# Optimization experiments

Measured on AMD Instinct MI355X. Metric: run time of the kernel, lower is better.

Reference implementation:

```python
import jax, jax.numpy as jnp
import numpy as np

B, N, DIM, K, H, R = 128, 196, 384, 16, 6, 4  # batch, tokens, channels, bases, heads, adapter ratio


def setup_inputs() -> dict:
    key = jax.random.key(0)
    ks = jax.random.split(key, 4)
    d_r = DIM // R
    return {
        "x": jax.random.normal(ks[0], (B, N, DIM), jnp.float32),
        "W1": jax.random.normal(ks[1], (DIM, d_r), jnp.float32) * 0.02,
        "b1": jnp.zeros((d_r,), jnp.float32),
        "W2": jax.random.normal(ks[2], (d_r, K * H), jnp.float32) * 0.02,
        "b2": jnp.zeros((K * H,), jnp.float32),
        "weight_bank": jax.random.normal(ks[3], (K, N, N), jnp.float32) * 0.02,
    }


def reference(x, W1, b1, W2, b2, weight_bank):
    Bsz, n, C = x.shape
    hdim = C // H
    # adapter MLP: Linear -> GELU(exact/erf, torch default) -> Linear
    hid = jax.nn.gelu(x @ W1 + b1, approximate=False)
    mix = (hid @ W2 + b2).reshape(Bsz, n, K, H)
    # mode='softmax': normalize mixing policy over the k bases
    mix = jax.nn.softmax(mix, axis=2)
    # dynamic per-sample token-mixing matrix [B, n, n, H]
    weight = jnp.einsum('bnkh,knm->bnmh', mix, weight_bank)
    # mix tokens: contract over source token index n
    xh = x.reshape(Bsz, n, H, hdim)
    out = jnp.einsum('bnhc,bnmh->bmhc', xh, weight).reshape(Bsz, n, C)
    return out
```

## Files before the change

kernel.cpp:

```cpp
#include <hip/hip_runtime.h>
#include <math.h>

#define BB  128
#define NN  196
#define CDIM 384
#define KK  16
#define HH  6
#define DR  96
#define HD  64

typedef __attribute__((ext_vector_type(8))) short bf16x8;
typedef __attribute__((ext_vector_type(4))) float f32x4;

__device__ __forceinline__ unsigned short f2bf(float f) {
    unsigned u = __float_as_uint(f);
    u += 0x7FFFu + ((u >> 16) & 1u);
    return (unsigned short)(u >> 16);
}
__device__ __forceinline__ unsigned pk2bf(float lo, float hi) {
    return (unsigned)f2bf(lo) | ((unsigned)f2bf(hi) << 16);
}
__device__ __forceinline__ float bflo(unsigned u) { return __uint_as_float(u << 16); }
__device__ __forceinline__ float bfhi(unsigned u) { return __uint_as_float(u & 0xFFFF0000u); }

union AFrag { unsigned u[4]; bf16x8 f; };

__global__ __launch_bounds__(128) void prep_kernel(
    const float* __restrict__ W1, const float* __restrict__ W2,
    unsigned short* __restrict__ W1T, unsigned short* __restrict__ W2T)
{
    const int c = blockIdx.x;
    const int t = threadIdx.x;
    for (int k = t; k < CDIM; k += 128)
        W1T[(size_t)c * CDIM + k] = f2bf(W1[(size_t)k * DR + c]);
    if (t < DR)
        W2T[(size_t)c * DR + t] = f2bf(W2[(size_t)t * DR + c]);
}

__global__ __launch_bounds__(256, 3) void adapter_kernel(
    const float* __restrict__ x,   const unsigned short* __restrict__ W1T,
    const float* __restrict__ b1,  const unsigned short* __restrict__ W2T,
    const float* __restrict__ b2,  unsigned short* __restrict__ mix_out)
{
    __shared__ unsigned short hidb[32][104];

    const int t    = threadIdx.x;
    const int w    = t >> 6;
    const int wm   = w & 1;
    const int wc   = w >> 1;
    const int lane = t & 63;
    const int l15  = lane & 15;
    const int lq   = lane >> 4;
    const int row0 = blockIdx.x * 32;

    f32x4 acc[3];
    #pragma unroll
    for (int ct = 0; ct < 3; ++ct) {
        const float bj = b1[wc * 48 + ct * 16 + l15];
        acc[ct] = (f32x4){bj, bj, bj, bj};
    }
    const float* xrow = x + (size_t)(row0 + wm * 16 + l15) * CDIM;
    for (int kc = 0; kc < CDIM; kc += 32) {
        const float4 u = *(const float4*)(xrow + kc + 8 * lq);
        const float4 v = *(const float4*)(xrow + kc + 8 * lq + 4);
        AFrag af;
        af.u[0] = pk2bf(u.x, u.y); af.u[1] = pk2bf(u.z, u.w);
        af.u[2] = pk2bf(v.x, v.y); af.u[3] = pk2bf(v.z, v.w);
        #pragma unroll
        for (int ct = 0; ct < 3; ++ct) {
            const bf16x8 bf = *(const bf16x8*)(W1T + (size_t)(wc * 48 + ct * 16 + l15) * CDIM + kc + 8 * lq);
            acc[ct] = __builtin_amdgcn_mfma_f32_16x16x32_bf16(af.f, bf, acc[ct], 0, 0, 0);
        }
    }
    #pragma unroll
    for (int ct = 0; ct < 3; ++ct)
        #pragma unroll
        for (int r = 0; r < 4; ++r) {
            const float vv = acc[ct][r];
            hidb[wm * 16 + lq * 4 + r][wc * 48 + ct * 16 + l15] =
                f2bf(0.5f * vv * (1.0f + erff(vv * 0.70710678118654752f)));
        }
    __syncthreads();

    f32x4 acc2[3];
    #pragma unroll
    for (int ct = 0; ct < 3; ++ct) {
        const float bj = b2[wc * 48 + ct * 16 + l15];
        acc2[ct] = (f32x4){bj, bj, bj, bj};
    }
    #pragma unroll
    for (int kc = 0; kc < DR; kc += 32) {
        const bf16x8 af = *(const bf16x8*)&hidb[wm * 16 + l15][kc + 8 * lq];
        #pragma unroll
        for (int ct = 0; ct < 3; ++ct) {
            const bf16x8 bf = *(const bf16x8*)(W2T + (size_t)(wc * 48 + ct * 16 + l15) * DR + kc + 8 * lq);
            acc2[ct] = __builtin_amdgcn_mfma_f32_16x16x32_bf16(af, bf, acc2[ct], 0, 0, 0);
        }
    }
    __syncthreads();

    #pragma unroll
    for (int ct = 0; ct < 3; ++ct)
        #pragma unroll
        for (int r = 0; r < 4; ++r)
            hidb[wm * 16 + lq * 4 + r][wc * 48 + ct * 16 + l15] = f2bf(acc2[ct][r]);
    __syncthreads();

    if (t < 192) {
        const int r = t / 6, h = t % 6;
        float lg[KK];
        float mx = -1e30f;
        #pragma unroll
        for (int k = 0; k < KK; ++k) {
            lg[k] = __uint_as_float((unsigned)hidb[r][6 * k + h] << 16);
            mx = fmaxf(mx, lg[k]);
        }
        float s = 0.f;
        #pragma unroll
        for (int k = 0; k < KK; ++k) { lg[k] = __expf(lg[k] - mx); s += lg[k]; }
        const float inv = 1.0f / s;
        unsigned o[8];
        #pragma unroll
        for (int jj = 0; jj < 8; ++jj)
            o[jj] = pk2bf(lg[2 * jj] * inv, lg[2 * jj + 1] * inv);
        unsigned* op = (unsigned*)(mix_out + ((size_t)(row0 + r) * HH + h) * KK);
        *(uint4*)op       = make_uint4(o[0], o[1], o[2], o[3]);
        *(uint4*)(op + 4) = make_uint4(o[4], o[5], o[6], o[7]);
    }
}

__global__ __launch_bounds__(384, 3) void mix_mfma_kernel(
    const float* __restrict__ x,  const unsigned short* __restrict__ mixb,
    const float* __restrict__ wb, float* __restrict__ out)
{
    __shared__ unsigned short xT[CDIM][40];
    __shared__ unsigned short Asb[HH][64][40];
    __shared__ unsigned short msc[32][96];

    const int t   = threadIdx.x;
    const int bid = blockIdx.x;
    const int q   = bid & 3;
    const int b   = bid >> 2;
    const int m0  = q * 52;
    const int qvalid = (q == 3) ? 40 : 52;
    const int h   = t >> 6;
    const int lane = t & 63;
    const int l15 = lane & 15;
    const int lq  = lane >> 4;

    f32x4 acc[4][4];
    #pragma unroll
    for (int mt = 0; mt < 4; ++mt)
        #pragma unroll
        for (int ct = 0; ct < 4; ++ct) acc[mt][ct] = (f32x4){0.f, 0.f, 0.f, 0.f};

    for (int nc = 0; nc < 7; ++nc) {
        const int n0 = nc * 32;
        __syncthreads();

        #pragma unroll
        for (int it = 0; it < 4; ++it) {
            const int task = t + 384 * it;
            const int p  = task & 15;
            const int cq = task >> 4;
            const int n  = n0 + 2 * p;
            float4 va = make_float4(0.f, 0.f, 0.f, 0.f);
            float4 vb = make_float4(0.f, 0.f, 0.f, 0.f);
            if (n < NN)     va = *(const float4*)(x + ((size_t)b * NN + n) * CDIM + 4 * cq);
            if (n + 1 < NN) vb = *(const float4*)(x + ((size_t)b * NN + n + 1) * CDIM + 4 * cq);
            *(unsigned*)&xT[4 * cq + 0][2 * p] = pk2bf(va.x, vb.x);
            *(unsigned*)&xT[4 * cq + 1][2 * p] = pk2bf(va.y, vb.y);
            *(unsigned*)&xT[4 * cq + 2][2 * p] = pk2bf(va.z, vb.z);
            *(unsigned*)&xT[4 * cq + 3][2 * p] = pk2bf(va.w, vb.w);
        }
        #pragma unroll
        for (int it = 0; it < 4; ++it) {
            const int idx = t + 384 * it;
            const int nl = idx / 48, cw = idx - nl * 48;
            unsigned v = 0u;
            if (n0 + nl < NN)
                v = *(const unsigned*)(mixb + ((size_t)b * NN + n0 + nl) * DR + 2 * cw);
            *(unsigned*)&msc[nl][2 * cw] = v;
        }
        __syncthreads();

        for (int task = t; task < 832; task += 384) {
            const int nl = task / 26;
            const int mp = task - nl * 26;
            const int n  = n0 + nl;
            const int ms = 2 * mp;
            if (n < NN && ms < qvalid) {
                const int m = m0 + ms;
                float2 wv[KK];
                #pragma unroll
                for (int k = 0; k < KK; ++k)
                    wv[k] = *(const float2*)(wb + ((size_t)k * NN + n) * NN + m);
                #pragma unroll
                for (int hh = 0; hh < HH; ++hh) {
                    const uint4 u = *(const uint4*)&msc[nl][hh * 16];
                    const uint4 v = *(const uint4*)&msc[nl][hh * 16 + 8];
                    const unsigned uu[8] = {u.x, u.y, u.z, u.w, v.x, v.y, v.z, v.w};
                    float a0 = 0.f, a1 = 0.f;
                    #pragma unroll
                    for (int p = 0; p < 8; ++p) {
                        const float f0 = bflo(uu[p]), f1 = bfhi(uu[p]);
                        a0 += f0 * wv[2 * p].x;     a1 += f0 * wv[2 * p].y;
                        a0 += f1 * wv[2 * p + 1].x; a1 += f1 * wv[2 * p + 1].y;
                    }
                    Asb[hh][ms][nl]     = f2bf(a0);
                    Asb[hh][ms + 1][nl] = f2bf(a1);
                }
            } else {
                #pragma unroll
                for (int hh = 0; hh < HH; ++hh) {
                    Asb[hh][ms][nl] = 0; Asb[hh][ms + 1][nl] = 0;
                }
            }
        }
        __syncthreads();

        bf16x8 afr[4], bfr[4];
        #pragma unroll
        for (int mt = 0; mt < 4; ++mt)
            afr[mt] = *(const bf16x8*)&Asb[h][mt * 16 + l15][8 * lq];
        #pragma unroll
        for (int ct = 0; ct < 4; ++ct)
            bfr[ct] = *(const bf16x8*)&xT[h * HD + ct * 16 + l15][8 * lq];
        #pragma unroll
        for (int mt = 0; mt < 4; ++mt)
            #pragma unroll
            for (int ct = 0; ct < 4; ++ct)
                acc[mt][ct] = __builtin_amdgcn_mfma_f32_16x16x32_bf16(
                    afr[mt], bfr[ct], acc[mt][ct], 0, 0, 0);
    }

    #pragma unroll
    for (int mt = 0; mt < 4; ++mt) {
        #pragma unroll
        for (int r = 0; r < 4; ++r) {
            const int ms = mt * 16 + lq * 4 + r;
            if (ms < qvalid) {
                float* op = out + ((size_t)b * NN + m0 + ms) * CDIM + h * HD + l15;
                #pragma unroll
                for (int ct = 0; ct < 4; ++ct)
                    op[ct * 16] = acc[mt][ct][r];
            }
        }
    }
}

extern "C" void kernel_launch(void* const* d_in, const int* in_sizes, int n_in,
                              void* d_out, int out_size, void* d_ws, size_t ws_size,
                              hipStream_t stream) {
    (void)in_sizes; (void)n_in; (void)out_size; (void)ws_size;
    const float* x  = (const float*)d_in[0];
    const float* W1 = (const float*)d_in[1];
    const float* b1 = (const float*)d_in[2];
    const float* W2 = (const float*)d_in[3];
    const float* b2 = (const float*)d_in[4];
    const float* wb = (const float*)d_in[5];
    float* out = (float*)d_out;

    unsigned short* mixbuf = (unsigned short*)d_ws;
    unsigned short* w1t = (unsigned short*)((char*)d_ws + 4816896);
    unsigned short* w2t = (unsigned short*)((char*)d_ws + 4890624);

    prep_kernel<<<96, 128, 0, stream>>>(W1, W2, w1t, w2t);
    adapter_kernel<<<(BB * NN) / 32, 256, 0, stream>>>(x, w1t, b1, w2t, b2, mixbuf);
    mix_mfma_kernel<<<4 * BB, 384, 0, stream>>>(x, mixbuf, wb, out);
}
```

Baseline: 224.4 us.

## Compute dynamic mixing weights with MFMA from a transposed bf16 weight bank

```diff
diff --git a/kernel.cpp b/kernel.cpp
--- a/kernel.cpp
+++ b/kernel.cpp
@@ -20,38 +20,54 @@
 __device__ __forceinline__ unsigned pk2bf(float lo, float hi) {
     return (unsigned)f2bf(lo) | ((unsigned)f2bf(hi) << 16);
 }
-__device__ __forceinline__ float bflo(unsigned u) { return __uint_as_float(u << 16); }
-__device__ __forceinline__ float bfhi(unsigned u) { return __uint_as_float(u & 0xFFFF0000u); }
 
 union AFrag { unsigned u[4]; bf16x8 f; };
 
-__global__ __launch_bounds__(128) void prep_kernel(
+__global__ __launch_bounds__(256) void prep_kernel(
     const float* __restrict__ W1, const float* __restrict__ W2,
-    unsigned short* __restrict__ W1T, unsigned short* __restrict__ W2T)
+    const float* __restrict__ wb,
+    unsigned short* __restrict__ W1T, unsigned short* __restrict__ W2T,
+    unsigned short* __restrict__ wbT)
 {
-    const int c = blockIdx.x;
-    const int t = threadIdx.x;
-    for (int k = t; k < CDIM; k += 128)
-        W1T[(size_t)c * CDIM + k] = f2bf(W1[(size_t)k * DR + c]);
-    if (t < DR)
-        W2T[(size_t)c * DR + t] = f2bf(W2[(size_t)t * DR + c]);
-}
-
-__global__ __launch_bounds__(256, 3) void adapter_kernel(
+    const int bid = blockIdx.x;
+    const int t   = threadIdx.x;
+    if (bid < DR) {
+        const int c = bid;
+        for (int k = t; k < CDIM; k += 256)
+            W1T[(size_t)c * CDIM + k] = f2bf(W1[(size_t)k * DR + c]);
+        if (t < DR)
+            W2T[(size_t)c * DR + t] = f2bf(W2[(size_t)t * DR + c]);
+    } else {
+        const int n = bid - DR;
+        const int m = t;
+        if (m < NN) {
+            unsigned o[8];
+            #pragma unroll
+            for (int j = 0; j < 8; ++j) {
+                const float a = wb[((size_t)(2 * j)     * NN + n) * NN + m];
+                const float c = wb[((size_t)(2 * j + 1) * NN + n) * NN + m];
+                o[j] = pk2bf(a, c);
+            }
+            unsigned* dst = (unsigned*)(wbT + ((size_t)n * NN + m) * KK);
+            *(uint4*)dst       = make_uint4(o[0], o[1], o[2], o[3]);
+            *(uint4*)(dst + 4) = make_uint4(o[4], o[5], o[6], o[7]);
+        }
+    }
+}
+
+__global__ __launch_bounds__(128, 3) void adapter_kernel(
     const float* __restrict__ x,   const unsigned short* __restrict__ W1T,
     const float* __restrict__ b1,  const unsigned short* __restrict__ W2T,
     const float* __restrict__ b2,  unsigned short* __restrict__ mix_out)
 {
-    __shared__ unsigned short hidb[32][104];
+    __shared__ unsigned short hidb[16][104];
 
     const int t    = threadIdx.x;
-    const int w    = t >> 6;
-    const int wm   = w & 1;
-    const int wc   = w >> 1;
+    const int wc   = t >> 6;
     const int lane = t & 63;
     const int l15  = lane & 15;
     const int lq   = lane >> 4;
-    const int row0 = blockIdx.x * 32;
+    const int row0 = blockIdx.x * 16;
 
     f32x4 acc[3];
     #pragma unroll
@@ -59,7 +75,7 @@
         const float bj = b1[wc * 48 + ct * 16 + l15];
         acc[ct] = (f32x4){bj, bj, bj, bj};
     }
-    const float* xrow = x + (size_t)(row0 + wm * 16 + l15) * CDIM;
+    const float* xrow = x + (size_t)(row0 + l15) * CDIM;
     for (int kc = 0; kc < CDIM; kc += 32) {
         const float4 u = *(const float4*)(xrow + kc + 8 * lq);
         const float4 v = *(const float4*)(xrow + kc + 8 * lq + 4);
@@ -77,7 +93,7 @@
         #pragma unroll
         for (int r = 0; r < 4; ++r) {
             const float vv = acc[ct][r];
-            hidb[wm * 16 + lq * 4 + r][wc * 48 + ct * 16 + l15] =
+            hidb[lq * 4 + r][wc * 48 + ct * 16 + l15] =
                 f2bf(0.5f * vv * (1.0f + erff(vv * 0.70710678118654752f)));
         }
     __syncthreads();
@@ -90,7 +106,7 @@
     }
     #pragma unroll
     for (int kc = 0; kc < DR; kc += 32) {
-        const bf16x8 af = *(const bf16x8*)&hidb[wm * 16 + l15][kc + 8 * lq];
+        const bf16x8 af = *(const bf16x8*)&hidb[l15][kc + 8 * lq];
         #pragma unroll
         for (int ct = 0; ct < 3; ++ct) {
             const bf16x8 bf = *(const bf16x8*)(W2T + (size_t)(wc * 48 + ct * 16 + l15) * DR + kc + 8 * lq);
@@ -103,10 +119,10 @@
     for (int ct = 0; ct < 3; ++ct)
         #pragma unroll
         for (int r = 0; r < 4; ++r)
-            hidb[wm * 16 + lq * 4 + r][wc * 48 + ct * 16 + l15] = f2bf(acc2[ct][r]);
+            hidb[lq * 4 + r][wc * 48 + ct * 16 + l15] = f2bf(acc2[ct][r]);
     __syncthreads();
 
-    if (t < 192) {
+    if (t < 96) {
         const int r = t / 6, h = t % 6;
         float lg[KK];
         float mx = -1e30f;
@@ -129,30 +145,36 @@
     }
 }
 
-__global__ __launch_bounds__(384, 3) void mix_mfma_kernel(
+__global__ __launch_bounds__(192, 3) void mix_mfma_kernel(
     const float* __restrict__ x,  const unsigned short* __restrict__ mixb,
-    const float* __restrict__ wb, float* __restrict__ out)
+    const unsigned short* __restrict__ wbT, float* __restrict__ out)
 {
-    __shared__ unsigned short xT[CDIM][40];
-    __shared__ unsigned short Asb[HH][64][40];
-    __shared__ unsigned short msc[32][96];
-
-    const int t   = threadIdx.x;
-    const int bid = blockIdx.x;
-    const int q   = bid & 3;
-    const int b   = bid >> 2;
-    const int m0  = q * 52;
+    __shared__ unsigned short xT[192][40];
+    __shared__ unsigned short Asb[3][64][40];
+
+    const int t    = threadIdx.x;
+    const int bid  = blockIdx.x;
+    const int b    = bid & 127;
+    const int sub  = bid >> 7;
+    const int q    = sub >> 1;
+    const int hp   = sub & 1;
+    const int m0   = q * 52;
     const int qvalid = (q == 3) ? 40 : 52;
-    const int h   = t >> 6;
+    const int lw   = t >> 6;
+    const int hbase = hp * 3;
     const int lane = t & 63;
-    const int l15 = lane & 15;
-    const int lq  = lane >> 4;
+    const int l15  = lane & 15;
+    const int lq   = lane >> 4;
+    const int c0   = hp * 192;
+
+    const bf16x8 z8 = {0, 0, 0, 0, 0, 0, 0, 0};
+    const f32x4  cz = {0.f, 0.f, 0.f, 0.f};
 
     f32x4 acc[4][4];
     #pragma unroll
     for (int mt = 0; mt < 4; ++mt)
         #pragma unroll
-        for (int ct = 0; ct < 4; ++ct) acc[mt][ct] = (f32x4){0.f, 0.f, 0.f, 0.f};
+        for (int ct = 0; ct < 4; ++ct) acc[mt][ct] = cz;
 
     for (int nc = 0; nc < 7; ++nc) {
         const int n0 = nc * 32;
@@ -160,61 +182,49 @@
 
         #pragma unroll
         for (int it = 0; it < 4; ++it) {
-            const int task = t + 384 * it;
+            const int task = t + 192 * it;
             const int p  = task & 15;
             const int cq = task >> 4;
             const int n  = n0 + 2 * p;
             float4 va = make_float4(0.f, 0.f, 0.f, 0.f);
             float4 vb = make_float4(0.f, 0.f, 0.f, 0.f);
-            if (n < NN)     va = *(const float4*)(x + ((size_t)b * NN + n) * CDIM + 4 * cq);
-            if (n + 1 < NN) vb = *(const float4*)(x + ((size_t)b * NN + n + 1) * CDIM + 4 * cq);
+            if (n < NN)     va = *(const float4*)(x + ((size_t)b * NN + n) * CDIM + c0 + 4 * cq);
+            if (n + 1 < NN) vb = *(const float4*)(x + ((size_t)b * NN + n + 1) * CDIM + c0 + 4 * cq);
             *(unsigned*)&xT[4 * cq + 0][2 * p] = pk2bf(va.x, vb.x);
             *(unsigned*)&xT[4 * cq + 1][2 * p] = pk2bf(va.y, vb.y);
             *(unsigned*)&xT[4 * cq + 2][2 * p] = pk2bf(va.z, vb.z);
             *(unsigned*)&xT[4 * cq + 3][2 * p] = pk2bf(va.w, vb.w);
         }
-        #pragma unroll
-        for (int it = 0; it < 4; ++it) {
-            const int idx = t + 384 * it;
-            const int nl = idx / 48, cw = idx - nl * 48;
-            unsigned v = 0u;
-            if (n0 + nl < NN)
-                v = *(const unsigned*)(mixb + ((size_t)b * NN + n0 + nl) * DR + 2 * cw);
-            *(unsigned*)&msc[nl][2 * cw] = v;
-        }
-        __syncthreads();
-
-        for (int task = t; task < 832; task += 384) {
-            const int nl = task / 26;
-            const int mp = task - nl * 26;
-            const int n  = n0 + nl;
-            const int ms = 2 * mp;
-            if (n < NN && ms < qvalid) {
-                const int m = m0 + ms;
-                float2 wv[KK];
+
+        for (int nl = lw; nl < 32; nl += 3) {
+            const int n = n0 + nl;
+            if (n < NN) {
+                bf16x8 af = z8;
+                if (l15 < HH && lq < 2)
+                    af = *(const bf16x8*)(mixb + (((size_t)b * NN + n) * HH + l15) * KK + 8 * lq);
                 #pragma unroll
-                for (int k = 0; k < KK; ++k)
-                    wv[k] = *(const float2*)(wb + ((size_t)k * NN + n) * NN + m);
-                #pragma unroll
-                for (int hh = 0; hh < HH; ++hh) {
-                    const uint4 u = *(const uint4*)&msc[nl][hh * 16];
-                    const uint4 v = *(const uint4*)&msc[nl][hh * 16 + 8];
-                    const unsigned uu[8] = {u.x, u.y, u.z, u.w, v.x, v.y, v.z, v.w};
-                    float a0 = 0.f, a1 = 0.f;
+                for (int mt = 0; mt < 4; ++mt) {
+                    const int m = m0 + mt * 16 + l15;
+                    bf16x8 bf = z8;
+                    if (lq < 2 && m < NN)
+                        bf = *(const bf16x8*)(wbT + ((size_t)n * NN + m) * KK + 8 * lq);
+                    const f32x4 c = __builtin_amdgcn_mfma_f32_16x16x32_bf16(af, bf, cz, 0, 0, 0);
                     #pragma unroll
-                    for (int p = 0; p < 8; ++p) {
-                        const float f0 = bflo(uu[p]), f1 = bfhi(uu[p]);
-                        a0 += f0 * wv[2 * p].x;     a1 += f0 * wv[2 * p].y;
-                        a0 += f1 * wv[2 * p + 1].x; a1 += f1 * wv[2 * p + 1].y;
+                    for (int r = 0; r < 4; ++r) {
+                        const int hh = lq * 4 + r;
+                        if (hh >= hbase && hh < hbase + 3)
+                            Asb[hh - hbase][mt * 16 + l15][nl] = f2bf(c[r]);
                     }
-                    Asb[hh][ms][nl]     = f2bf(a0);
-                    Asb[hh][ms + 1][nl] = f2bf(a1);
                 }
             } else {
                 #pragma unroll
-                for (int hh = 0; hh < HH; ++hh) {
-                    Asb[hh][ms][nl] = 0; Asb[hh][ms + 1][nl] = 0;
-                }
+                for (int mt = 0; mt < 4; ++mt)
+                    #pragma unroll
+                    for (int r = 0; r < 4; ++r) {
+                        const int hh = lq * 4 + r;
+                        if (hh >= hbase && hh < hbase + 3)
+                            Asb[hh - hbase][mt * 16 + l15][nl] = 0;
+                    }
             }
         }
         __syncthreads();
@@ -222,10 +232,10 @@
         bf16x8 afr[4], bfr[4];
         #pragma unroll
         for (int mt = 0; mt < 4; ++mt)
-            afr[mt] = *(const bf16x8*)&Asb[h][mt * 16 + l15][8 * lq];
+            afr[mt] = *(const bf16x8*)&Asb[lw][mt * 16 + l15][8 * lq];
         #pragma unroll
         for (int ct = 0; ct < 4; ++ct)
-            bfr[ct] = *(const bf16x8*)&xT[h * HD + ct * 16 + l15][8 * lq];
+            bfr[ct] = *(const bf16x8*)&xT[lw * 64 + ct * 16 + l15][8 * lq];
         #pragma unroll
         for (int mt = 0; mt < 4; ++mt)
             #pragma unroll
@@ -234,6 +244,7 @@
                     afr[mt], bfr[ct], acc[mt][ct], 0, 0, 0);
     }
 
+    const int h = hbase + lw;
     #pragma unroll
     for (int mt = 0; mt < 4; ++mt) {
         #pragma unroll
@@ -264,8 +275,9 @@
     unsigned short* mixbuf = (unsigned short*)d_ws;
     unsigned short* w1t = (unsigned short*)((char*)d_ws + 4816896);
     unsigned short* w2t = (unsigned short*)((char*)d_ws + 4890624);
-
-    prep_kernel<<<96, 128, 0, stream>>>(W1, W2, w1t, w2t);
-    adapter_kernel<<<(BB * NN) / 32, 256, 0, stream>>>(x, w1t, b1, w2t, b2, mixbuf);
-    mix_mfma_kernel<<<4 * BB, 384, 0, stream>>>(x, mixbuf, wb, out);
-}
+    unsigned short* wbt = (unsigned short*)((char*)d_ws + 4909056);
+
+    prep_kernel<<<DR + NN, 256, 0, stream>>>(W1, W2, wb, w1t, w2t, wbt);
+    adapter_kernel<<<(BB * NN) / 16, 128, 0, stream>>>(x, w1t, b1, w2t, b2, mixbuf);
+    mix_mfma_kernel<<<8 * BB, 192, 0, stream>>>(x, mixbuf, wbt, out);
+}
```

Result: slower. 240.4 us (+7.1%).
